# Performance work log

Measured on AMD Instinct MI355X. Metric: run time of the kernel, lower is better.

## Reference

```python
import jax, jax.numpy as jnp
import numpy as np

EPS = 1e-5  # torch LayerNorm default eps
L2_EPS = 1e-12


def _l2norm(t, axis=-1):
    return t / jnp.sqrt(jnp.sum(t * t, axis=axis, keepdims=True) + L2_EPS)


def setup_inputs() -> dict:
    key = jax.random.key(0)
    k1, k2, k3 = jax.random.split(key, 3)
    b, n, d = 4, 2048, 1024
    h, e, cs = 8, 16, 2048
    x = jax.random.normal(k1, (b, n, d), dtype=jnp.float32)
    # xavier_normal_ on [h, d, e]: fan_in = d*e, fan_out = h*e
    std = float(np.sqrt(2.0 / (d * e + h * e)))
    rand_projs = jax.random.normal(k2, (h, d, e), dtype=jnp.float32) * std
    codebook = jax.random.normal(k3, (h, cs, e), dtype=jnp.float32)
    return {"x": x, "rand_projs": rand_projs, "codebook": codebook}


def reference(x, rand_projs, codebook):
    # LayerNorm over last dim, no affine
    mu = jnp.mean(x, axis=-1, keepdims=True)
    var = jnp.mean((x - mu) ** 2, axis=-1, keepdims=True)
    xn = (x - mu) / jnp.sqrt(var + EPS)
    # per-head random projection: [b,n,d] x [h,d,e] -> [b,n,h,e]
    proj = jnp.einsum('bnd,hde->bnhe', xn, rand_projs)
    # cosine-sim VQ per head: normalize both, argmax similarity
    q = _l2norm(proj, axis=-1)                 # [b,n,h,e]
    cb = _l2norm(codebook, axis=-1)            # [h,c,e]
    sim = jnp.einsum('bnhe,hce->bnhc', q, cb)  # [b,n,h,c]
    indices = jnp.argmax(sim, axis=-1)         # [b,n,h] int
    return indices
```

## Files before the change

### kernel.cpp

```cpp
#include <hip/hip_runtime.h>
#include <math.h>


typedef short bf16x8 __attribute__((ext_vector_type(8)));
typedef float f32x4 __attribute__((ext_vector_type(4)));

__device__ __forceinline__ unsigned short f2bf(float f) {
  unsigned u = __builtin_bit_cast(unsigned, f);
  unsigned r = (u + 0x7FFFu + ((u >> 16) & 1u)) >> 16;
  return (unsigned short)r;
}
__device__ __forceinline__ float bf2f(unsigned short b) {
  return __builtin_bit_cast(float, (unsigned)b << 16);
}
__device__ __forceinline__ void split3(float v, unsigned short& h,
                                       unsigned short& m, unsigned short& l) {
  h = f2bf(v);
  float r = v - bf2f(h);
  m = f2bf(r);
  float r2 = r - bf2f(m);
  l = f2bf(r2);
}

__global__ __launch_bounds__(256) void k_cbnorm(const float* __restrict__ cb,
                                                unsigned short* __restrict__ cfrag) {
  int v = blockIdx.x * 256 + threadIdx.x;
  int h = v >> 11, c = v & 2047, tl = c >> 4, n = c & 15;
  const float4* p = (const float4*)(cb + (size_t)v * 16);
  float4 q0 = p[0], q1 = p[1], q2 = p[2], q3 = p[3];
  float f[16] = {q0.x,q0.y,q0.z,q0.w, q1.x,q1.y,q1.z,q1.w,
                 q2.x,q2.y,q2.z,q2.w, q3.x,q3.y,q3.z,q3.w};
  double s = 0.0;
#pragma unroll
  for (int i = 0; i < 16; ++i) s += (double)f[i] * (double)f[i];
  double inv = 1.0 / sqrt(s + 1e-12);
  __attribute__((aligned(16))) unsigned short vp[3][16];
#pragma unroll
  for (int i = 0; i < 16; ++i)
    split3((float)((double)f[i] * inv), vp[0][i], vp[1][i], vp[2][i]);
#pragma unroll
  for (int pp = 0; pp < 3; ++pp) {
    size_t base = ((((size_t)h * 128 + tl) * 3 + pp) * 16 + n) * 16;
    ((bf16x8*)(cfrag + base))[0] = ((bf16x8*)vp[pp])[0];
    ((bf16x8*)(cfrag + base))[1] = ((bf16x8*)vp[pp])[1];
  }
}

__global__ __launch_bounds__(256) void k_colsum(const float* __restrict__ W,
                                                float* __restrict__ cs) {
  __shared__ float red[16][17];
  int h = blockIdx.x;
  int e = threadIdx.x & 15, part = threadIdx.x >> 4;
  const float* base = W + h * 16384 + e;
  float s = 0.f;
  int d0 = part * 64;
  for (int i = 0; i < 64; ++i) s += base[(d0 + i) * 16];
  red[e][part] = s;
  __syncthreads();
  if (threadIdx.x < 16) {
    float t = 0.f;
#pragma unroll
    for (int p = 0; p < 16; ++p) t += red[threadIdx.x][p];
    cs[h * 16 + threadIdx.x] = t;
  }
}

__global__ __launch_bounds__(256) void k_wsplit(const float* __restrict__ W,
                                                unsigned short* __restrict__ wfrag) {
  int id = blockIdx.x * 256 + threadIdx.x;
  int o = id & 1, n = (id >> 1) & 15, c = (id >> 5) & 7, dg = id >> 8;
  __attribute__((aligned(16))) unsigned short vp[3][8];
#pragma unroll
  for (int j = 0; j < 8; ++j) {
    float v = W[c * 16384 + (dg * 16 + o * 8 + j) * 16 + n];
    split3(v, vp[0][j], vp[1][j], vp[2][j]);
  }
#pragma unroll
  for (int pp = 0; pp < 3; ++pp) {
    size_t base = ((((size_t)dg * 8 + c) * 3 + pp) * 16 + n) * 16 + o * 8;
    *(bf16x8*)(wfrag + base) = *(bf16x8*)vp[pp];
  }
}

__global__ __launch_bounds__(256) void k_proj(const float* __restrict__ x,
                                              const unsigned short* __restrict__ wfrag,
                                              float* __restrict__ part,
                                              float* __restrict__ psum) {
  const int t = threadIdx.x;
  const int lane = t & 63, w = t >> 6;
  const int r0 = blockIdx.x * 128;
  const int ks = blockIdx.y;
  const int q = lane >> 4, n16 = lane & 15, oct = q & 1;
  const bool qlt2 = (q < 2);
  const int p1 = qlt2 ? 0 : 1, p2 = qlt2 ? 1 : 0, p3 = qlt2 ? 2 : 0;

  f32x4 acc[2][8];
#pragma unroll
  for (int mt = 0; mt < 2; ++mt)
#pragma unroll
    for (int h = 0; h < 8; ++h) acc[mt][h] = (f32x4){0.f, 0.f, 0.f, 0.f};
  float ps[2] = {0.f, 0.f};

  for (int dg = 0; dg < 8; ++dg) {
    const int dq = ks * 128 + dg * 16 + oct * 8;
    bf16x8 a1[2], a3[2];
#pragma unroll
    for (int mt = 0; mt < 2; ++mt) {
      const int row = r0 + w * 32 + mt * 16 + n16;
      float4 xa = *(const float4*)(x + (size_t)row * 1024 + dq);
      float4 xb = *(const float4*)(x + (size_t)row * 1024 + dq + 4);
      float xf[8] = {xa.x, xa.y, xa.z, xa.w, xb.x, xb.y, xb.z, xb.w};
      ps[mt] += ((xf[0] + xf[1]) + (xf[2] + xf[3])) +
                ((xf[4] + xf[5]) + (xf[6] + xf[7]));
      __attribute__((aligned(16))) unsigned short s1[8], s3[8];
#pragma unroll
      for (int j = 0; j < 8; ++j) {
        unsigned short hh, mm, ll;
        split3(xf[j], hh, mm, ll);
        s1[j] = qlt2 ? hh : mm;
        s3[j] = qlt2 ? hh : ll;
      }
      a1[mt] = *(bf16x8*)s1;
      a3[mt] = *(bf16x8*)s3;
    }
#pragma unroll
    for (int hh = 0; hh < 8; ++hh) {
      size_t b0 = (((size_t)((ks * 8 + dg) * 8 + hh) * 3) * 16 + n16) * 16 + oct * 8;
      bf16x8 b1 = *(const bf16x8*)(wfrag + b0 + p1 * 256);
      bf16x8 b2 = *(const bf16x8*)(wfrag + b0 + p2 * 256);
      bf16x8 b3 = *(const bf16x8*)(wfrag + b0 + p3 * 256);
#pragma unroll
      for (int mt = 0; mt < 2; ++mt) {
        acc[mt][hh] = __builtin_amdgcn_mfma_f32_16x16x32_bf16(a1[mt], b1, acc[mt][hh], 0, 0, 0);
        acc[mt][hh] = __builtin_amdgcn_mfma_f32_16x16x32_bf16(a1[mt], b2, acc[mt][hh], 0, 0, 0);
        acc[mt][hh] = __builtin_amdgcn_mfma_f32_16x16x32_bf16(a3[mt], b3, acc[mt][hh], 0, 0, 0);
      }
    }
  }

  float* po = part + ((size_t)ks * 8192 + r0 + w * 32) * 128;
#pragma unroll
  for (int mt = 0; mt < 2; ++mt)
#pragma unroll
    for (int hh = 0; hh < 8; ++hh)
#pragma unroll
      for (int r = 0; r < 4; ++r)
        po[(size_t)(mt * 16 + q * 4 + r) * 128 + hh * 16 + n16] = acc[mt][hh][r];

  float pr0 = ps[0] + __shfl_xor(ps[0], 16);
  float pr1 = ps[1] + __shfl_xor(ps[1], 16);
  if (lane < 16) {
    psum[(size_t)ks * 8192 + r0 + w * 32 + n16] = pr0;
    psum[(size_t)ks * 8192 + r0 + w * 32 + 16 + n16] = pr1;
  }
}

__global__ __launch_bounds__(256) void k_combine(const float* __restrict__ part,
                                                 const float* __restrict__ psum,
                                                 const float* __restrict__ csum,
                                                 unsigned short* __restrict__ ph,
                                                 unsigned short* __restrict__ pm,
                                                 unsigned short* __restrict__ pl) {
  int idx = blockIdx.x * 256 + threadIdx.x;
  int row = idx >> 5, c4 = (idx & 31) * 4;
  float4 a = {0.f, 0.f, 0.f, 0.f};
  float msum = 0.f;
#pragma unroll
  for (int s = 0; s < 8; ++s) {
    float4 p = *(const float4*)(part + ((size_t)s * 8192 + row) * 128 + c4);
    a.x += p.x; a.y += p.y; a.z += p.z; a.w += p.w;
    msum += psum[(size_t)s * 8192 + row];
  }
  float m = msum * (1.0f / 1024.0f);
  float4 cs = *(const float4*)(csum + c4);
  float o[4] = {a.x - m * cs.x, a.y - m * cs.y, a.z - m * cs.z, a.w - m * cs.w};
  __attribute__((aligned(8))) unsigned short vh[4], vm[4], vl[4];
#pragma unroll
  for (int k = 0; k < 4; ++k) split3(o[k], vh[k], vm[k], vl[k]);
  int head = c4 >> 4, e0 = c4 & 15;
  size_t base = ((size_t)head * 8192 + row) * 16 + e0;
  *(short4*)(ph + base) = *(short4*)vh;
  *(short4*)(pm + base) = *(short4*)vm;
  *(short4*)(pl + base) = *(short4*)vl;
}

__global__ __launch_bounds__(256) void k_argmax(
    const unsigned short* __restrict__ ph, const unsigned short* __restrict__ pm,
    const unsigned short* __restrict__ pl, const unsigned short* __restrict__ cfrag,
    float* __restrict__ amv, int* __restrict__ ami) {
  const int t = threadIdx.x;
  const int lane = t & 63, w = t >> 6;
  const int h = blockIdx.y;
  const int z = blockIdx.z;
  const int r0 = blockIdx.x * 512 + w * 128;
  const int q = lane >> 4, n16 = lane & 15;
  const int ehalf = (q & 1) * 8;
  const bool qlt2 = (q < 2);
  const int p1 = qlt2 ? 0 : 1, p2 = qlt2 ? 1 : 0, p3 = qlt2 ? 2 : 0;

  const unsigned short* pa1 = qlt2 ? ph : pm;
  const unsigned short* pa3 = qlt2 ? ph : pl;
  bf16x8 a1[8], a3[8];
#pragma unroll
  for (int rt = 0; rt < 8; ++rt) {
    size_t off = ((size_t)h * 8192 + r0 + rt * 16 + n16) * 16 + ehalf;
    a1[rt] = *(const bf16x8*)(pa1 + off);
    a3[rt] = *(const bf16x8*)(pa3 + off);
  }

  float best[8][4];
  int   bidx[8][4];
#pragma unroll
  for (int rt = 0; rt < 8; ++rt)
#pragma unroll
    for (int r = 0; r < 4; ++r) { best[rt][r] = -3.402823466e38f; bidx[rt][r] = 0; }

  for (int tile = 0; tile < 32; ++tile) {
    size_t b0 = ((((size_t)h * 128 + z * 32 + tile) * 3) * 16 + n16) * 16 + ehalf;
    bf16x8 b1 = *(const bf16x8*)(cfrag + b0 + p1 * 256);
    bf16x8 b2 = *(const bf16x8*)(cfrag + b0 + p2 * 256);
    bf16x8 b3 = *(const bf16x8*)(cfrag + b0 + p3 * 256);
    const int code = z * 512 + tile * 16 + n16;
#pragma unroll
    for (int rt = 0; rt < 8; ++rt) {
      f32x4 acc = {0.f, 0.f, 0.f, 0.f};
      acc = __builtin_amdgcn_mfma_f32_16x16x32_bf16(a1[rt], b1, acc, 0, 0, 0);
      acc = __builtin_amdgcn_mfma_f32_16x16x32_bf16(a1[rt], b2, acc, 0, 0, 0);
      acc = __builtin_amdgcn_mfma_f32_16x16x32_bf16(a3[rt], b3, acc, 0, 0, 0);
#pragma unroll
      for (int r = 0; r < 4; ++r)
        if (acc[r] > best[rt][r]) { best[rt][r] = acc[r]; bidx[rt][r] = code; }
    }
  }

#pragma unroll
  for (int off = 8; off >= 1; off >>= 1) {
#pragma unroll
    for (int rt = 0; rt < 8; ++rt)
#pragma unroll
      for (int r = 0; r < 4; ++r) {
        float ov = __shfl_xor(best[rt][r], off, 16);
        int   oi = __shfl_xor(bidx[rt][r], off, 16);
        if (ov > best[rt][r] || (ov == best[rt][r] && oi < bidx[rt][r])) {
          best[rt][r] = ov; bidx[rt][r] = oi;
        }
      }
  }
  if (n16 == 0) {
#pragma unroll
    for (int rt = 0; rt < 8; ++rt)
#pragma unroll
      for (int r = 0; r < 4; ++r) {
        int row = r0 + rt * 16 + q * 4 + r;
        size_t o = (size_t)z * 65536 + (size_t)row * 8 + h;
        amv[o] = best[rt][r]; ami[o] = bidx[rt][r];
      }
  }
}

__global__ __launch_bounds__(256) void k_amred(const float* __restrict__ amv,
                                               const int* __restrict__ ami,
                                               int* __restrict__ out) {
  int i = blockIdx.x * 256 + threadIdx.x;
  float bv = amv[i]; int bi = ami[i];
#pragma unroll
  for (int z = 1; z < 4; ++z) {
    float v = amv[(size_t)z * 65536 + i];
    if (v > bv) { bv = v; bi = ami[(size_t)z * 65536 + i]; }
  }
  out[i] = bi;
}

extern "C" void kernel_launch(void* const* d_in, const int* in_sizes, int n_in,
                              void* d_out, int out_size, void* d_ws, size_t ws_size,
                              hipStream_t stream) {
  (void)in_sizes; (void)n_in; (void)out_size; (void)ws_size;
  const float* x  = (const float*)d_in[0];
  const float* rp = (const float*)d_in[1];
  const float* cb = (const float*)d_in[2];
  int* out = (int*)d_out;

  float* ws = (float*)d_ws;
  float*          csum  = ws;
  float*          psum  = ws + 128;
  float*          part  = ws + 65664;
  float*          amv   = ws + 8454272;
  int*            ami   = (int*)(ws + 8716416);
  unsigned short* wfrag = (unsigned short*)(ws + 8978560);
  unsigned short* cfrag = (unsigned short*)(ws + 9175168);
  unsigned short* ph    = (unsigned short*)(ws + 9568384);
  unsigned short* pm    = (unsigned short*)(ws + 10092672);
  unsigned short* pl    = (unsigned short*)(ws + 10616960);

  hipLaunchKernelGGL(k_cbnorm,  dim3(64),        dim3(256), 0, stream, cb, cfrag);
  hipLaunchKernelGGL(k_colsum,  dim3(8),         dim3(256), 0, stream, rp, csum);
  hipLaunchKernelGGL(k_wsplit,  dim3(64),        dim3(256), 0, stream, rp, wfrag);
  hipLaunchKernelGGL(k_proj,    dim3(64, 8),     dim3(256), 0, stream, x, wfrag, part, psum);
  hipLaunchKernelGGL(k_combine, dim3(1024),      dim3(256), 0, stream, part, psum, csum, ph, pm, pl);
  hipLaunchKernelGGL(k_argmax,  dim3(16, 8, 4),  dim3(256), 0, stream, ph, pm, pl, cfrag, amv, ami);
  hipLaunchKernelGGL(k_amred,   dim3(256),       dim3(256), 0, stream, amv, ami, out);
}
```

Baseline: 162.6 us.

## Fuse split-K combine into projection via LDS reduction; stage codebook tiles in LDS

The projection kernel now gives each block 16 rows over the full K range, with the four waves splitting K. It reduces their partials in shared memory and applies mean-centering plus the 3-way bf16 split in place. This removes the separate combine kernel and the large global partial-sum buffer. The argmax kernel now uses smaller row and code tiles with more z-splits, loads its codebook slice into LDS with global_load_lds, and the final reduction reads 8 partitions. The trade-offs are lower per-block MFMA reuse in the projection and more partial argmax traffic.

```diff
diff --git a/kernel.cpp b/kernel.cpp
--- a/kernel.cpp
+++ b/kernel.cpp
@@ -4,6 +4,12 @@
 
 typedef short bf16x8 __attribute__((ext_vector_type(8)));
 typedef float f32x4 __attribute__((ext_vector_type(4)));
+
+__device__ __forceinline__ void stage16(const float* g, float* lds_base) {
+  __builtin_amdgcn_global_load_lds(
+      (const __attribute__((address_space(1))) void*)g,
+      (__attribute__((address_space(3))) void*)lds_base, 16, 0, 0);
+}
 
 __device__ __forceinline__ unsigned short f2bf(float f) {
   unsigned u = __builtin_bit_cast(unsigned, f);
@@ -84,145 +90,139 @@
 
 __global__ __launch_bounds__(256) void k_proj(const float* __restrict__ x,
                                               const unsigned short* __restrict__ wfrag,
-                                              float* __restrict__ part,
-                                              float* __restrict__ psum) {
+                                              const float* __restrict__ csum,
+                                              unsigned short* __restrict__ ph,
+                                              unsigned short* __restrict__ pm,
+                                              unsigned short* __restrict__ pl) {
+  __shared__ float sAcc[4][64][33];
+  __shared__ float sPs[4][2][16];
+  __shared__ float sMu[16];
   const int t = threadIdx.x;
   const int lane = t & 63, w = t >> 6;
-  const int r0 = blockIdx.x * 128;
-  const int ks = blockIdx.y;
+  const int r0 = blockIdx.x * 16;
   const int q = lane >> 4, n16 = lane & 15, oct = q & 1;
   const bool qlt2 = (q < 2);
   const int p1 = qlt2 ? 0 : 1, p2 = qlt2 ? 1 : 0, p3 = qlt2 ? 2 : 0;
-
-  f32x4 acc[2][8];
-#pragma unroll
-  for (int mt = 0; mt < 2; ++mt)
-#pragma unroll
-    for (int h = 0; h < 8; ++h) acc[mt][h] = (f32x4){0.f, 0.f, 0.f, 0.f};
-  float ps[2] = {0.f, 0.f};
-
-  for (int dg = 0; dg < 8; ++dg) {
-    const int dq = ks * 128 + dg * 16 + oct * 8;
-    bf16x8 a1[2], a3[2];
-#pragma unroll
-    for (int mt = 0; mt < 2; ++mt) {
-      const int row = r0 + w * 32 + mt * 16 + n16;
-      float4 xa = *(const float4*)(x + (size_t)row * 1024 + dq);
-      float4 xb = *(const float4*)(x + (size_t)row * 1024 + dq + 4);
-      float xf[8] = {xa.x, xa.y, xa.z, xa.w, xb.x, xb.y, xb.z, xb.w};
-      ps[mt] += ((xf[0] + xf[1]) + (xf[2] + xf[3])) +
-                ((xf[4] + xf[5]) + (xf[6] + xf[7]));
-      __attribute__((aligned(16))) unsigned short s1[8], s3[8];
-#pragma unroll
-      for (int j = 0; j < 8; ++j) {
-        unsigned short hh, mm, ll;
-        split3(xf[j], hh, mm, ll);
-        s1[j] = qlt2 ? hh : mm;
-        s3[j] = qlt2 ? hh : ll;
-      }
-      a1[mt] = *(bf16x8*)s1;
-      a3[mt] = *(bf16x8*)s3;
-    }
+  const int row = r0 + n16;
+
+  f32x4 acc[8];
+#pragma unroll
+  for (int h = 0; h < 8; ++h) acc[h] = (f32x4){0.f, 0.f, 0.f, 0.f};
+  float ps = 0.f;
+
+  for (int dg2 = 0; dg2 < 16; ++dg2) {
+    const int dg = w * 16 + dg2;
+    const int dq = dg * 16 + oct * 8;
+    float4 xa = *(const float4*)(x + (size_t)row * 1024 + dq);
+    float4 xb = *(const float4*)(x + (size_t)row * 1024 + dq + 4);
+    float xf[8] = {xa.x, xa.y, xa.z, xa.w, xb.x, xb.y, xb.z, xb.w};
+    ps += ((xf[0] + xf[1]) + (xf[2] + xf[3])) +
+          ((xf[4] + xf[5]) + (xf[6] + xf[7]));
+    __attribute__((aligned(16))) unsigned short s1[8], s3[8];
+#pragma unroll
+    for (int j = 0; j < 8; ++j) {
+      unsigned short hh, mm, ll;
+      split3(xf[j], hh, mm, ll);
+      s1[j] = qlt2 ? hh : mm;
+      s3[j] = qlt2 ? hh : ll;
+    }
+    bf16x8 a1 = *(bf16x8*)s1;
+    bf16x8 a3 = *(bf16x8*)s3;
 #pragma unroll
     for (int hh = 0; hh < 8; ++hh) {
-      size_t b0 = (((size_t)((ks * 8 + dg) * 8 + hh) * 3) * 16 + n16) * 16 + oct * 8;
+      size_t b0 = (((size_t)(dg * 8 + hh) * 3) * 16 + n16) * 16 + oct * 8;
       bf16x8 b1 = *(const bf16x8*)(wfrag + b0 + p1 * 256);
       bf16x8 b2 = *(const bf16x8*)(wfrag + b0 + p2 * 256);
       bf16x8 b3 = *(const bf16x8*)(wfrag + b0 + p3 * 256);
-#pragma unroll
-      for (int mt = 0; mt < 2; ++mt) {
-        acc[mt][hh] = __builtin_amdgcn_mfma_f32_16x16x32_bf16(a1[mt], b1, acc[mt][hh], 0, 0, 0);
-        acc[mt][hh] = __builtin_amdgcn_mfma_f32_16x16x32_bf16(a1[mt], b2, acc[mt][hh], 0, 0, 0);
-        acc[mt][hh] = __builtin_amdgcn_mfma_f32_16x16x32_bf16(a3[mt], b3, acc[mt][hh], 0, 0, 0);
-      }
-    }
-  }
-
-  float* po = part + ((size_t)ks * 8192 + r0 + w * 32) * 128;
-#pragma unroll
-  for (int mt = 0; mt < 2; ++mt)
-#pragma unroll
-    for (int hh = 0; hh < 8; ++hh)
-#pragma unroll
-      for (int r = 0; r < 4; ++r)
-        po[(size_t)(mt * 16 + q * 4 + r) * 128 + hh * 16 + n16] = acc[mt][hh][r];
-
-  float pr0 = ps[0] + __shfl_xor(ps[0], 16);
-  float pr1 = ps[1] + __shfl_xor(ps[1], 16);
-  if (lane < 16) {
-    psum[(size_t)ks * 8192 + r0 + w * 32 + n16] = pr0;
-    psum[(size_t)ks * 8192 + r0 + w * 32 + 16 + n16] = pr1;
-  }
-}
-
-__global__ __launch_bounds__(256) void k_combine(const float* __restrict__ part,
-                                                 const float* __restrict__ psum,
-                                                 const float* __restrict__ csum,
-                                                 unsigned short* __restrict__ ph,
-                                                 unsigned short* __restrict__ pm,
-                                                 unsigned short* __restrict__ pl) {
-  int idx = blockIdx.x * 256 + threadIdx.x;
-  int row = idx >> 5, c4 = (idx & 31) * 4;
-  float4 a = {0.f, 0.f, 0.f, 0.f};
-  float msum = 0.f;
-#pragma unroll
-  for (int s = 0; s < 8; ++s) {
-    float4 p = *(const float4*)(part + ((size_t)s * 8192 + row) * 128 + c4);
-    a.x += p.x; a.y += p.y; a.z += p.z; a.w += p.w;
-    msum += psum[(size_t)s * 8192 + row];
-  }
-  float m = msum * (1.0f / 1024.0f);
-  float4 cs = *(const float4*)(csum + c4);
-  float o[4] = {a.x - m * cs.x, a.y - m * cs.y, a.z - m * cs.z, a.w - m * cs.w};
-  __attribute__((aligned(8))) unsigned short vh[4], vm[4], vl[4];
-#pragma unroll
-  for (int k = 0; k < 4; ++k) split3(o[k], vh[k], vm[k], vl[k]);
-  int head = c4 >> 4, e0 = c4 & 15;
-  size_t base = ((size_t)head * 8192 + row) * 16 + e0;
-  *(short4*)(ph + base) = *(short4*)vh;
-  *(short4*)(pm + base) = *(short4*)vm;
-  *(short4*)(pl + base) = *(short4*)vl;
+      acc[hh] = __builtin_amdgcn_mfma_f32_16x16x32_bf16(a1, b1, acc[hh], 0, 0, 0);
+      acc[hh] = __builtin_amdgcn_mfma_f32_16x16x32_bf16(a1, b2, acc[hh], 0, 0, 0);
+      acc[hh] = __builtin_amdgcn_mfma_f32_16x16x32_bf16(a3, b3, acc[hh], 0, 0, 0);
+    }
+  }
+
+#pragma unroll
+  for (int hh = 0; hh < 8; ++hh)
+#pragma unroll
+    for (int r = 0; r < 4; ++r) sAcc[w][lane][hh * 4 + r] = acc[hh][r];
+  if (q < 2) sPs[w][q][n16] = ps;
+  __syncthreads();
+  if (t < 16) {
+    float s = 0.f;
+#pragma unroll
+    for (int w2 = 0; w2 < 4; ++w2) s += sPs[w2][0][t] + sPs[w2][1][t];
+    sMu[t] = s * (1.0f / 1024.0f);
+  }
+  __syncthreads();
+
+  const int l = t & 63, g = t >> 6;
+  const int lq = l >> 4, ln = l & 15;
+#pragma unroll
+  for (int hh2 = 0; hh2 < 2; ++hh2) {
+    const int head = g * 2 + hh2;
+    const float cs = csum[head * 16 + ln];
+#pragma unroll
+    for (int r = 0; r < 4; ++r) {
+      const int f = head * 4 + r;
+      float v = ((sAcc[0][l][f] + sAcc[1][l][f]) +
+                 (sAcc[2][l][f] + sAcc[3][l][f]));
+      const int row16 = lq * 4 + r;
+      float tv = v - sMu[row16] * cs;
+      unsigned short vh, vm, vl;
+      split3(tv, vh, vm, vl);
+      size_t base = ((size_t)head * 8192 + r0 + row16) * 16 + ln;
+      ph[base] = vh; pm[base] = vm; pl[base] = vl;
+    }
+  }
 }
 
 __global__ __launch_bounds__(256) void k_argmax(
     const unsigned short* __restrict__ ph, const unsigned short* __restrict__ pm,
     const unsigned short* __restrict__ pl, const unsigned short* __restrict__ cfrag,
     float* __restrict__ amv, int* __restrict__ ami) {
+  __shared__ __align__(16) unsigned short sB[12288];
   const int t = threadIdx.x;
   const int lane = t & 63, w = t >> 6;
   const int h = blockIdx.y;
   const int z = blockIdx.z;
-  const int r0 = blockIdx.x * 512 + w * 128;
+  const int r0 = blockIdx.x * 256 + w * 64;
   const int q = lane >> 4, n16 = lane & 15;
   const int ehalf = (q & 1) * 8;
   const bool qlt2 = (q < 2);
   const int p1 = qlt2 ? 0 : 1, p2 = qlt2 ? 1 : 0, p3 = qlt2 ? 2 : 0;
 
+  const float* src = (const float*)(cfrag + ((size_t)(h * 128 + z * 16) * 3) * 256);
+#pragma unroll
+  for (int i = 0; i < 6; ++i)
+    stage16(src + ((size_t)((i * 4 + w) * 64) + lane) * 4,
+            (float*)sB + (i * 4 + w) * 256);
+
   const unsigned short* pa1 = qlt2 ? ph : pm;
   const unsigned short* pa3 = qlt2 ? ph : pl;
-  bf16x8 a1[8], a3[8];
-#pragma unroll
-  for (int rt = 0; rt < 8; ++rt) {
+  bf16x8 a1[4], a3[4];
+#pragma unroll
+  for (int rt = 0; rt < 4; ++rt) {
     size_t off = ((size_t)h * 8192 + r0 + rt * 16 + n16) * 16 + ehalf;
     a1[rt] = *(const bf16x8*)(pa1 + off);
     a3[rt] = *(const bf16x8*)(pa3 + off);
   }
 
-  float best[8][4];
-  int   bidx[8][4];
-#pragma unroll
-  for (int rt = 0; rt < 8; ++rt)
+  float best[4][4];
+  int   bidx[4][4];
+#pragma unroll
+  for (int rt = 0; rt < 4; ++rt)
 #pragma unroll
     for (int r = 0; r < 4; ++r) { best[rt][r] = -3.402823466e38f; bidx[rt][r] = 0; }
 
-  for (int tile = 0; tile < 32; ++tile) {
-    size_t b0 = ((((size_t)h * 128 + z * 32 + tile) * 3) * 16 + n16) * 16 + ehalf;
-    bf16x8 b1 = *(const bf16x8*)(cfrag + b0 + p1 * 256);
-    bf16x8 b2 = *(const bf16x8*)(cfrag + b0 + p2 * 256);
-    bf16x8 b3 = *(const bf16x8*)(cfrag + b0 + p3 * 256);
-    const int code = z * 512 + tile * 16 + n16;
-#pragma unroll
-    for (int rt = 0; rt < 8; ++rt) {
+  __syncthreads();
+
+  for (int tile = 0; tile < 16; ++tile) {
+    const int b0 = tile * 768 + n16 * 16 + ehalf;
+    bf16x8 b1 = *(const bf16x8*)(sB + b0 + p1 * 256);
+    bf16x8 b2 = *(const bf16x8*)(sB + b0 + p2 * 256);
+    bf16x8 b3 = *(const bf16x8*)(sB + b0 + p3 * 256);
+    const int code = z * 256 + tile * 16 + n16;
+#pragma unroll
+    for (int rt = 0; rt < 4; ++rt) {
       f32x4 acc = {0.f, 0.f, 0.f, 0.f};
       acc = __builtin_amdgcn_mfma_f32_16x16x32_bf16(a1[rt], b1, acc, 0, 0, 0);
       acc = __builtin_amdgcn_mfma_f32_16x16x32_bf16(a1[rt], b2, acc, 0, 0, 0);
@@ -236,7 +236,7 @@
 #pragma unroll
   for (int off = 8; off >= 1; off >>= 1) {
 #pragma unroll
-    for (int rt = 0; rt < 8; ++rt)
+    for (int rt = 0; rt < 4; ++rt)
 #pragma unroll
       for (int r = 0; r < 4; ++r) {
         float ov = __shfl_xor(best[rt][r], off, 16);
@@ -248,7 +248,7 @@
   }
   if (n16 == 0) {
 #pragma unroll
-    for (int rt = 0; rt < 8; ++rt)
+    for (int rt = 0; rt < 4; ++rt)
 #pragma unroll
       for (int r = 0; r < 4; ++r) {
         int row = r0 + rt * 16 + q * 4 + r;
@@ -264,7 +264,7 @@
   int i = blockIdx.x * 256 + threadIdx.x;
   float bv = amv[i]; int bi = ami[i];
 #pragma unroll
-  for (int z = 1; z < 4; ++z) {
+  for (int z = 1; z < 8; ++z) {
     float v = amv[(size_t)z * 65536 + i];
     if (v > bv) { bv = v; bi = ami[(size_t)z * 65536 + i]; }
   }
@@ -282,21 +282,18 @@
 
   float* ws = (float*)d_ws;
   float*          csum  = ws;
-  float*          psum  = ws + 128;
-  float*          part  = ws + 65664;
-  float*          amv   = ws + 8454272;
-  int*            ami   = (int*)(ws + 8716416);
-  unsigned short* wfrag = (unsigned short*)(ws + 8978560);
-  unsigned short* cfrag = (unsigned short*)(ws + 9175168);
-  unsigned short* ph    = (unsigned short*)(ws + 9568384);
-  unsigned short* pm    = (unsigned short*)(ws + 10092672);
-  unsigned short* pl    = (unsigned short*)(ws + 10616960);
+  float*          amv   = ws + 128;
+  int*            ami   = (int*)(ws + 524416);
+  unsigned short* wfrag = (unsigned short*)(ws + 1048704);
+  unsigned short* cfrag = (unsigned short*)(ws + 1245312);
+  unsigned short* ph    = (unsigned short*)(ws + 1638528);
+  unsigned short* pm    = (unsigned short*)(ws + 2162816);
+  unsigned short* pl    = (unsigned short*)(ws + 2687104);
 
   hipLaunchKernelGGL(k_cbnorm,  dim3(64),        dim3(256), 0, stream, cb, cfrag);
   hipLaunchKernelGGL(k_colsum,  dim3(8),         dim3(256), 0, stream, rp, csum);
   hipLaunchKernelGGL(k_wsplit,  dim3(64),        dim3(256), 0, stream, rp, wfrag);
-  hipLaunchKernelGGL(k_proj,    dim3(64, 8),     dim3(256), 0, stream, x, wfrag, part, psum);
-  hipLaunchKernelGGL(k_combine, dim3(1024),      dim3(256), 0, stream, part, psum, csum, ph, pm, pl);
-  hipLaunchKernelGGL(k_argmax,  dim3(16, 8, 4),  dim3(256), 0, stream, ph, pm, pl, cfrag, amv, ami);
+  hipLaunchKernelGGL(k_proj,    dim3(512),       dim3(256), 0, stream, x, wfrag, csum, ph, pm, pl);
+  hipLaunchKernelGGL(k_argmax,  dim3(32, 8, 8),  dim3(256), 0, stream, ph, pm, pl, cfrag, amv, ami);
   hipLaunchKernelGGL(k_amred,   dim3(256),       dim3(256), 0, stream, amv, ami, out);
 }
```

Measured after the change: 161.1 us. About the same (-0.9%).
